# Kernel tuning notes

Measured on AMD Instinct MI355X. Metric: run time of the kernel, lower is better.

## Reference

```python
import jax, jax.numpy as jnp
import numpy as np

B, E, H, KVH, S = 1, 4096, 32, 8, 2048
HD = E // H            # per-head dim = 128
KVE = KVH * HD         # kv projection embed dim = 1024


def setup_inputs() -> dict:
    key = jax.random.key(0)
    ks = jax.random.split(key, 10)
    std = 0.02
    return {
        "input_embeds": jax.random.normal(ks[0], (B, E, 1, S), jnp.float32),
        "cos": jax.random.uniform(ks[1], (HD, S), jnp.float32, -1.0, 1.0),
        "sin": jax.random.uniform(ks[2], (HD, S), jnp.float32, -1.0, 1.0),
        "wq": jax.random.normal(ks[3], (E, E), jnp.float32) * std,
        "bq": jnp.zeros((E,), jnp.float32),
        "wk": jax.random.normal(ks[4], (KVE, E), jnp.float32) * std,
        "wv": jax.random.normal(ks[5], (KVE, E), jnp.float32) * std,
        "bv": jnp.zeros((KVE,), jnp.float32),
        "wo": jax.random.normal(ks[6], (E, E), jnp.float32) * std,
        "bo": jnp.zeros((E,), jnp.float32),
    }


def _proj(w, x, b=None):
    # 1x1 Conv2d == channelwise linear on (B, C, 1, S)
    y = jnp.einsum('oc,bcxs->boxs', w, x)
    if b is not None:
        y = y + b[None, :, None, None]
    return y


def _rope(x, cos, sin):
    # x: (B, h, HD, S); rotate-half along head_dim axis
    half = x.shape[2] // 2
    x1, x2 = x[:, :, :half], x[:, :, half:]
    rot = jnp.concatenate([-x2, x1], axis=2)
    return x * cos[None, None] + rot * sin[None, None]


def reference(input_embeds, cos, sin, wq, bq, wk, wv, bv, wo, bo):
    b, e, _, s = input_embeds.shape
    hd = e // H
    q = _proj(wq, input_embeds, bq)          # (B, E, 1, S)
    k = _proj(wk, input_embeds)              # (B, KVE, 1, S)  (no bias)
    v = _proj(wv, input_embeds, bv)          # (B, KVE, 1, S)

    qh = q.reshape(b, H, hd, s)
    kh = k.reshape(b, KVH, hd, s)
    qh = _rope(qh, cos, sin)
    kh = _rope(kh, cos, sin)

    # GQA tiling: channel-block repeat => query head h uses kv head (h % KVH)
    rep = H // KVH
    kfull = jnp.tile(kh, (1, rep, 1, 1))                       # (B, H, HD, S)
    vfull = jnp.tile(v.reshape(b, KVH, hd, s), (1, rep, 1, 1))  # (B, H, HD, S)

    scale = 1.0 / np.sqrt(hd).astype(np.float32)
    scores = jnp.einsum('bhcq,bhck->bhqk', qh, kfull) * scale  # (B, H, S, S)
    causal = jnp.tril(jnp.ones((s, s), bool))
    scores = jnp.where(causal[None, None], scores, jnp.finfo(scores.dtype).min)
    w = jax.nn.softmax(scores, axis=-1)
    attn = jnp.einsum('bhqk,bhck->bhcq', w, vfull).reshape(b, e, 1, s)
    return _proj(wo, attn, bo)
```

## Files before the change

### kernel.cpp

```cpp
#include <hip/hip_runtime.h>


typedef unsigned short u16;
typedef unsigned int u32;
typedef __attribute__((ext_vector_type(8))) short bf16x8;
typedef __attribute__((ext_vector_type(4))) float f32x4;

__device__ __forceinline__ u16 f2b(float f){
  union { float f; u32 u; } v; v.f = f;
  u32 r = (v.u + 0x7FFFu + ((v.u >> 16) & 1u)) >> 16;
  return (u16)r;
}
__device__ __forceinline__ float b2f(u16 b){
  union { u32 u; float f; } v; v.u = ((u32)b) << 16;
  return v.f;
}

__device__ __forceinline__ void gld16(const void* g, void* l){
  __builtin_amdgcn_global_load_lds((const __attribute__((address_space(1))) u32*)g,
                                   (__attribute__((address_space(3))) u32*)l, 16, 0, 0);
}

__global__ __launch_bounds__(256) void cvt_w(const float* __restrict__ src,
                                             u16* __restrict__ dst, int n4)
{
  int i = blockIdx.x * 256 + threadIdx.x;
  if (i < n4){
    float4 v = *(const float4*)&src[(size_t)i * 4];
    ushort4 o; o.x = f2b(v.x); o.y = f2b(v.y); o.z = f2b(v.z); o.w = f2b(v.w);
    *(ushort4*)&dst[(size_t)i * 4] = o;
  }
}

__global__ __launch_bounds__(256) void transpose_x(const float* __restrict__ X,
                                                   u16* __restrict__ XT)
{
  __shared__ float lds[64][65];
  const int c0 = blockIdx.x * 64, s0 = blockIdx.y * 64;
  const int tid = threadIdx.x;
  {
    const int sg = tid & 15, cl = tid >> 4;
#pragma unroll
    for (int p = 0; p < 4; ++p){
      int c = cl + p * 16;
      float4 v = *(const float4*)&X[(size_t)(c0 + c) * 2048 + s0 + sg * 4];
      lds[sg*4+0][c] = v.x; lds[sg*4+1][c] = v.y;
      lds[sg*4+2][c] = v.z; lds[sg*4+3][c] = v.w;
    }
  }
  __syncthreads();
  {
    const int cg = tid & 15, sl = tid >> 4;
#pragma unroll
    for (int p = 0; p < 4; ++p){
      int s = sl + p * 16;
      ushort4 o;
      o.x = f2b(lds[s][cg*4+0]); o.y = f2b(lds[s][cg*4+1]);
      o.z = f2b(lds[s][cg*4+2]); o.w = f2b(lds[s][cg*4+3]);
      *(ushort4*)&XT[(size_t)(s0 + s) * 4096 + c0 + cg * 4] = o;
    }
  }
}

template<int EPI, int ABF>
__global__ __launch_bounds__(256) void gemm2(
    const u16* __restrict__ W0, const u16* __restrict__ W1, const u16* __restrict__ W2,
    const float* __restrict__ F0, const float* __restrict__ F1, const float* __restrict__ F2,
    const u16* __restrict__ B,
    const float* __restrict__ bias0, const float* __restrict__ bias2,
    u16* __restrict__ QTo, u16* __restrict__ KTo, u16* __restrict__ Vno,
    float* __restrict__ OUT)
{
  const int K = 4096;
  const int m0 = blockIdx.y * 128, n0 = blockIdx.x * 128;

  const u16* A16; const float* Af; int mA;
  if (EPI == 0){
    if (m0 < 4096)      { A16 = W0; Af = F0; mA = m0; }
    else if (m0 < 5120) { A16 = W1; Af = F1; mA = m0 - 4096; }
    else                { A16 = W2; Af = F2; mA = m0 - 5120; }
  } else { A16 = W0; Af = F0; mA = m0; }

  __shared__ __align__(16) u16 As[128 * 32];
  __shared__ __align__(16) u16 Bs[128 * 32];

  const int tid = threadIdx.x, lane = tid & 63, w = tid >> 6;
  const int wm = w >> 1, wn = w & 1, quad = lane >> 4, l15 = lane & 15;

  f32x4 acc[4][4];
#pragma unroll
  for (int mt = 0; mt < 4; ++mt)
#pragma unroll
    for (int nt = 0; nt < 4; ++nt)
      acc[mt][nt] = f32x4{0.f, 0.f, 0.f, 0.f};

  const int r0 = tid >> 2, gs0 = tid & 3;
  const int g0 = gs0 ^ ((r0 >> 1) & 3);
  const int r1 = r0 + 64;

  u16* ldsA0 = As + (size_t)(w * 64) * 8;
  u16* ldsA1 = As + (size_t)(w * 64 + 256) * 8;
  u16* ldsB0 = Bs + (size_t)(w * 64) * 8;
  u16* ldsB1 = Bs + (size_t)(w * 64 + 256) * 8;

  const u16* bsrc0 = &B[(size_t)(n0 + r0) * 4096 + g0 * 8];
  const u16* bsrc1 = &B[(size_t)(n0 + r1) * 4096 + g0 * 8];
  const u16* asrc0 = ABF ? &A16[(size_t)(mA + r0) * 4096 + g0 * 8] : nullptr;
  const u16* asrc1 = ABF ? &A16[(size_t)(mA + r1) * 4096 + g0 * 8] : nullptr;
  const float* afs0 = ABF ? nullptr : &Af[(size_t)(mA + r0) * 4096 + g0 * 8];
  const float* afs1 = ABF ? nullptr : &Af[(size_t)(mA + r1) * 4096 + g0 * 8];

  int aoff[4], boff[4];
#pragma unroll
  for (int mt = 0; mt < 4; ++mt){
    int row = wm * 64 + mt * 16 + l15;
    aoff[mt] = row * 32 + (quad ^ ((row >> 1) & 3)) * 8;
  }
#pragma unroll
  for (int nt = 0; nt < 4; ++nt){
    int row = wn * 64 + nt * 16 + l15;
    boff[nt] = row * 32 + (quad ^ ((row >> 1) & 3)) * 8;
  }

  for (int kt = 0; kt < K / 32; ++kt){
    const int k0 = kt * 32;
    if (ABF){
      gld16(asrc0 + k0, ldsA0);
      gld16(asrc1 + k0, ldsA1);
    } else {
      float4 v0 = *(const float4*)&afs0[k0];
      float4 v1 = *(const float4*)&afs0[k0 + 4];
      float4 v2 = *(const float4*)&afs1[k0];
      float4 v3 = *(const float4*)&afs1[k0 + 4];
      union { u16 u[8]; uint4 q; } p0, p1;
      p0.u[0]=f2b(v0.x); p0.u[1]=f2b(v0.y); p0.u[2]=f2b(v0.z); p0.u[3]=f2b(v0.w);
      p0.u[4]=f2b(v1.x); p0.u[5]=f2b(v1.y); p0.u[6]=f2b(v1.z); p0.u[7]=f2b(v1.w);
      p1.u[0]=f2b(v2.x); p1.u[1]=f2b(v2.y); p1.u[2]=f2b(v2.z); p1.u[3]=f2b(v2.w);
      p1.u[4]=f2b(v3.x); p1.u[5]=f2b(v3.y); p1.u[6]=f2b(v3.z); p1.u[7]=f2b(v3.w);
      *(uint4*)&As[(size_t)tid * 8] = p0.q;
      *(uint4*)&As[(size_t)(tid + 256) * 8] = p1.q;
    }
    gld16(bsrc0 + k0, ldsB0);
    gld16(bsrc1 + k0, ldsB1);
    __syncthreads();

    bf16x8 af[4], bfr[4];
#pragma unroll
    for (int mt = 0; mt < 4; ++mt) af[mt]  = *(const bf16x8*)&As[aoff[mt]];
#pragma unroll
    for (int nt = 0; nt < 4; ++nt) bfr[nt] = *(const bf16x8*)&Bs[boff[nt]];
#pragma unroll
    for (int mt = 0; mt < 4; ++mt)
#pragma unroll
      for (int nt = 0; nt < 4; ++nt)
        acc[mt][nt] = __builtin_amdgcn_mfma_f32_16x16x32_bf16(af[mt], bfr[nt], acc[mt][nt], 0, 0, 0);
    __syncthreads();
  }

  if (EPI == 0){
    if (m0 < 4096){
#pragma unroll
      for (int mt = 0; mt < 4; ++mt){
        int mb = m0 + wm * 64 + mt * 16 + quad * 4;
        float b0 = bias0[mb], b1 = bias0[mb+1], b2 = bias0[mb+2], b3 = bias0[mb+3];
#pragma unroll
        for (int nt = 0; nt < 4; ++nt){
          int n = n0 + wn * 64 + nt * 16 + l15;
          ushort4 o;
          o.x = f2b(acc[mt][nt][0] + b0); o.y = f2b(acc[mt][nt][1] + b1);
          o.z = f2b(acc[mt][nt][2] + b2); o.w = f2b(acc[mt][nt][3] + b3);
          *(ushort4*)&QTo[(size_t)n * 4096 + mb] = o;
        }
      }
    } else if (m0 < 5120){
#pragma unroll
      for (int mt = 0; mt < 4; ++mt){
        int mb = m0 - 4096 + wm * 64 + mt * 16 + quad * 4;
#pragma unroll
        for (int nt = 0; nt < 4; ++nt){
          int n = n0 + wn * 64 + nt * 16 + l15;
          ushort4 o;
          o.x = f2b(acc[mt][nt][0]); o.y = f2b(acc[mt][nt][1]);
          o.z = f2b(acc[mt][nt][2]); o.w = f2b(acc[mt][nt][3]);
          *(ushort4*)&KTo[(size_t)n * 1024 + mb] = o;
        }
      }
    } else {
#pragma unroll
      for (int mt = 0; mt < 4; ++mt)
#pragma unroll
        for (int r = 0; r < 4; ++r){
          int mv = m0 - 5120 + wm * 64 + mt * 16 + quad * 4 + r;
          float bb = bias2[mv];
#pragma unroll
          for (int nt = 0; nt < 4; ++nt){
            int n = n0 + wn * 64 + nt * 16 + l15;
            Vno[(size_t)mv * 2048 + n] = f2b(acc[mt][nt][r] + bb);
          }
        }
    }
  } else {
#pragma unroll
    for (int mt = 0; mt < 4; ++mt)
#pragma unroll
      for (int r = 0; r < 4; ++r){
        int m = m0 + wm * 64 + mt * 16 + quad * 4 + r;
        float bb = bias0[m];
#pragma unroll
        for (int nt = 0; nt < 4; ++nt){
          int n = n0 + wn * 64 + nt * 16 + l15;
          OUT[(size_t)m * 2048 + n] = acc[mt][nt][r] + bb;
        }
      }
  }
}

__global__ __launch_bounds__(256) void rope_kernel(u16* __restrict__ QT,
                                                   u16* __restrict__ KT,
                                                   const float* __restrict__ cosp,
                                                   const float* __restrict__ sinp)
{
  const float qscale = 0.08838834764831845f * 1.4426950408889634f;
  int gid = blockIdx.x * 256 + threadIdx.x;
  const int NQ = 2048 * 32 * 64;
  if (gid < NQ){
    int c = gid & 63, hh = (gid >> 6) & 31, s = gid >> 11;
    size_t base = (size_t)s * 4096 + hh * 128 + c;
    float x1 = b2f(QT[base]), x2 = b2f(QT[base + 64]);
    float c1 = cosp[c * 2048 + s],        s1 = sinp[c * 2048 + s];
    float c2 = cosp[(c + 64) * 2048 + s], s2 = sinp[(c + 64) * 2048 + s];
    QT[base]      = f2b((x1 * c1 - x2 * s1) * qscale);
    QT[base + 64] = f2b((x2 * c2 + x1 * s2) * qscale);
  } else {
    int g = gid - NQ;
    int c = g & 63, hh = (g >> 6) & 7, s = g >> 9;
    size_t base = (size_t)s * 1024 + hh * 128 + c;
    float x1 = b2f(KT[base]), x2 = b2f(KT[base + 64]);
    float c1 = cosp[c * 2048 + s],        s1 = sinp[c * 2048 + s];
    float c2 = cosp[(c + 64) * 2048 + s], s2 = sinp[(c + 64) * 2048 + s];
    KT[base]      = f2b(x1 * c1 - x2 * s1);
    KT[base + 64] = f2b(x2 * c2 + x1 * s2);
  }
}

__global__ __launch_bounds__(256, 1) void attn3(const u16* __restrict__ QT,
                                                const u16* __restrict__ KT,
                                                const u16* __restrict__ Vn,
                                                u16* __restrict__ AT)
{
  const int h = blockIdx.x;
  const int p = blockIdx.y;
  const int kvh = h & 7;
  const int tid = threadIdx.x;
  const int w = tid >> 6, lane = tid & 63;
  const int quad = lane >> 4, l15 = lane & 15;

  const int k  = 4 * p + w;
  const int t1 = k, t2 = 63 - k;
  const int e1 = t1 >> 1, e2 = t2 >> 1;
  const int i01 = t1 * 32, i02 = t2 * 32;
  const int U = 32 - 2 * p;

  __shared__ __align__(16) u16 Ks[2][64 * 128];
  __shared__ __align__(16) u16 Vs[128 * 64];
  __shared__ __align__(16) u16 Ps[4][16][64];

  bf16x8 qa1[2][4], qa2[2][4];
#pragma unroll
  for (int mt = 0; mt < 2; ++mt)
#pragma unroll
    for (int kc = 0; kc < 4; ++kc){
      qa1[mt][kc] = *(const bf16x8*)&QT[(size_t)(i01 + mt * 16 + l15) * 4096
                                        + h * 128 + kc * 32 + quad * 8];
      qa2[mt][kc] = *(const bf16x8*)&QT[(size_t)(i02 + mt * 16 + l15) * 4096
                                        + h * 128 + kc * 32 + quad * 8];
    }

  f32x4 o1[2][9], o2[2][9];
#pragma unroll
  for (int mt = 0; mt < 2; ++mt)
#pragma unroll
    for (int ct = 0; ct < 9; ++ct){
      o1[mt][ct] = f32x4{0.f, 0.f, 0.f, 0.f};
      o2[mt][ct] = f32x4{0.f, 0.f, 0.f, 0.f};
    }

  bf16x8 ones;
#pragma unroll
  for (int z = 0; z < 8; ++z) ones[z] = (short)0x3F80;

  const int krl = lane >> 4, kgl = lane & 15;
  const int vrl = lane >> 3, vgl = lane & 7;

  auto stageK = [&](int buf, int j0){
#pragma unroll
    for (int q = 0; q < 4; ++q){
      int r = w * 16 + q * 4 + krl;
      gld16(&KT[(size_t)(j0 + r) * 1024 + kvh * 128 + ((kgl ^ (r & 7)) * 8)],
            &Ks[buf][(size_t)(w * 16 + q * 4) * 128]);
    }
  };
  auto stageV = [&](int j0){
#pragma unroll
    for (int q = 0; q < 4; ++q){
      int r = w * 32 + q * 8 + vrl;
      gld16(&Vn[(size_t)(kvh * 128 + r) * 2048 + j0 + ((vgl ^ (r & 7)) * 8)],
            &Vs[(size_t)(w * 32 + q * 8) * 64]);
    }
  };

  auto soft = [&](f32x4 (&s)[2][4], bf16x8 (&pa)[2][2], f32x4 (&o)[2][9],
                  int i0, int j0, bool maskit){
#pragma unroll
    for (int mt = 0; mt < 2; ++mt){
#pragma unroll
      for (int nt = 0; nt < 4; ++nt)
#pragma unroll
        for (int r = 0; r < 4; ++r){
          float pv = exp2f(fminf(s[mt][nt][r], 60.0f));
          if (maskit && (j0 + nt * 16 + l15 > i0 + mt * 16 + quad * 4 + r)) pv = 0.0f;
          int col = nt * 16 + l15, rowp = quad * 4 + r;
          Ps[w][rowp][((col >> 3) ^ (rowp & 7)) * 8 + (col & 7)] = f2b(pv);
        }
#pragma unroll
      for (int kc = 0; kc < 2; ++kc){
        pa[mt][kc] = *(const bf16x8*)&Ps[w][l15][((kc * 4 + quad) ^ (l15 & 7)) * 8];
        o[mt][8] = __builtin_amdgcn_mfma_f32_16x16x32_bf16(pa[mt][kc], ones, o[mt][8], 0, 0, 0);
      }
    }
  };

  auto epilogue = [&](f32x4 (&o)[2][9], int i0){
#pragma unroll
    for (int mt = 0; mt < 2; ++mt){
      float rinv[4];
#pragma unroll
      for (int r = 0; r < 4; ++r) rinv[r] = 1.0f / o[mt][8][r];
#pragma unroll
      for (int ct = 0; ct < 8; ++ct)
#pragma unroll
        for (int r = 0; r < 4; ++r){
          int i = i0 + mt * 16 + quad * 4 + r;
          AT[(size_t)i * 4096 + h * 128 + ct * 16 + l15] = f2b(o[mt][ct][r] * rinv[r]);
        }
    }
  };

  stageK(0, 0);
  for (int u = 0; u < U; ++u){
    __syncthreads();
    if (u + 1 < U) stageK((u + 1) & 1, (u + 1) * 64);
    stageV(u * 64);

    const int j0 = u * 64;
    const bool act1 = (u <= e1), act2 = (u <= e2);
    const u16* Kb = &Ks[u & 1][0];

    f32x4 s1[2][4], s2[2][4];
    bf16x8 pa1[2][2], pa2[2][2];
    if (act2 || act1){
#pragma unroll
      for (int mt = 0; mt < 2; ++mt)
#pragma unroll
        for (int nt = 0; nt < 4; ++nt){
          s1[mt][nt] = f32x4{0.f, 0.f, 0.f, 0.f};
          s2[mt][nt] = f32x4{0.f, 0.f, 0.f, 0.f};
        }
#pragma unroll
      for (int nt = 0; nt < 4; ++nt){
        bf16x8 kb[4];
#pragma unroll
        for (int kc = 0; kc < 4; ++kc){
          int row = nt * 16 + l15;
          kb[kc] = *(const bf16x8*)&Kb[row * 128 + (((kc * 4 + quad) ^ (row & 7)) * 8)];
        }
#pragma unroll
        for (int kc = 0; kc < 4; ++kc){
          s2[0][nt] = __builtin_amdgcn_mfma_f32_16x16x32_bf16(qa2[0][kc], kb[kc], s2[0][nt], 0, 0, 0);
          s2[1][nt] = __builtin_amdgcn_mfma_f32_16x16x32_bf16(qa2[1][kc], kb[kc], s2[1][nt], 0, 0, 0);
        }
        if (act1)
#pragma unroll
          for (int kc = 0; kc < 4; ++kc){
            s1[0][nt] = __builtin_amdgcn_mfma_f32_16x16x32_bf16(qa1[0][kc], kb[kc], s1[0][nt], 0, 0, 0);
            s1[1][nt] = __builtin_amdgcn_mfma_f32_16x16x32_bf16(qa1[1][kc], kb[kc], s1[1][nt], 0, 0, 0);
          }
      }
      if (act2) soft(s2, pa2, o2, i02, j0, u == e2);
      if (act1) soft(s1, pa1, o1, i01, j0, u == e1);
    }
    __syncthreads();

    if (act2 || act1){
#pragma unroll
      for (int ct = 0; ct < 8; ++ct)
#pragma unroll
        for (int kc = 0; kc < 2; ++kc){
          int row = ct * 16 + l15;
          bf16x8 vb = *(const bf16x8*)&Vs[row * 64 + (((kc * 4 + quad) ^ (row & 7)) * 8)];
          if (act2){
            o2[0][ct] = __builtin_amdgcn_mfma_f32_16x16x32_bf16(pa2[0][kc], vb, o2[0][ct], 0, 0, 0);
            o2[1][ct] = __builtin_amdgcn_mfma_f32_16x16x32_bf16(pa2[1][kc], vb, o2[1][ct], 0, 0, 0);
          }
          if (act1){
            o1[0][ct] = __builtin_amdgcn_mfma_f32_16x16x32_bf16(pa1[0][kc], vb, o1[0][ct], 0, 0, 0);
            o1[1][ct] = __builtin_amdgcn_mfma_f32_16x16x32_bf16(pa1[1][kc], vb, o1[1][ct], 0, 0, 0);
          }
        }
      if (u == e2) epilogue(o2, i02);
      if (u == e1) epilogue(o1, i01);
    }
  }
}

extern "C" void kernel_launch(void* const* d_in, const int* in_sizes, int n_in,
                              void* d_out, int out_size, void* d_ws, size_t ws_size,
                              hipStream_t stream)
{
  const float* X    = (const float*)d_in[0];
  const float* cosp = (const float*)d_in[1];
  const float* sinp = (const float*)d_in[2];
  const float* wq   = (const float*)d_in[3];
  const float* bq   = (const float*)d_in[4];
  const float* wk   = (const float*)d_in[5];
  const float* wv   = (const float*)d_in[6];
  const float* bv   = (const float*)d_in[7];
  const float* wo   = (const float*)d_in[8];
  const float* bo   = (const float*)d_in[9];
  float* out = (float*)d_out;

  char* ws = (char*)d_ws;
  const size_t MB = 1u << 20;

  if (ws_size >= 88 * MB){
    u16* W16Q = (u16*)(ws);
    u16* W16K = (u16*)(ws + 32 * MB);
    u16* W16V = (u16*)(ws + 40 * MB);
    u16* XT   = (u16*)(ws + 48 * MB);
    u16* QT   = (u16*)(ws + 64 * MB);
    u16* KT   = (u16*)(ws + 80 * MB);
    u16* Vn   = (u16*)(ws + 84 * MB);
    u16* AT   = (u16*)(ws + 48 * MB);
    u16* WO16 = (u16*)(ws);

    cvt_w<<<16384, 256, 0, stream>>>(wq, W16Q, 4194304);
    cvt_w<<< 4096, 256, 0, stream>>>(wk, W16K, 1048576);
    cvt_w<<< 4096, 256, 0, stream>>>(wv, W16V, 1048576);
    transpose_x<<<dim3(64, 32), 256, 0, stream>>>(X, XT);
    gemm2<0,1><<<dim3(16, 48), 256, 0, stream>>>(W16Q, W16K, W16V, wq, wk, wv,
                                                 XT, bq, bv, QT, KT, Vn, nullptr);
    cvt_w<<<16384, 256, 0, stream>>>(wo, WO16, 4194304);
    rope_kernel<<<20480, 256, 0, stream>>>(QT, KT, cosp, sinp);
    attn3<<<dim3(32, 8), 256, 0, stream>>>(QT, KT, Vn, AT);
    gemm2<1,1><<<dim3(16, 32), 256, 0, stream>>>(WO16, nullptr, nullptr, wo, nullptr, nullptr,
                                                 AT, bo, nullptr, nullptr, nullptr, nullptr, out);
  } else {
    u16* XT = (u16*)(ws);
    u16* QT = (u16*)(ws + 16 * MB);
    u16* KT = (u16*)(ws + 32 * MB);
    u16* Vn = (u16*)(ws + 36 * MB);
    u16* AT = (u16*)(ws + 40 * MB);

    transpose_x<<<dim3(64, 32), 256, 0, stream>>>(X, XT);
    gemm2<0,0><<<dim3(16, 48), 256, 0, stream>>>(nullptr, nullptr, nullptr, wq, wk, wv,
                                                 XT, bq, bv, QT, KT, Vn, nullptr);
    rope_kernel<<<20480, 256, 0, stream>>>(QT, KT, cosp, sinp);
    attn3<<<dim3(32, 8), 256, 0, stream>>>(QT, KT, Vn, AT);
    gemm2<1,0><<<dim3(16, 32), 256, 0, stream>>>(nullptr, nullptr, nullptr, wo, nullptr, nullptr,
                                                 AT, bo, nullptr, nullptr, nullptr, nullptr, out);
  }
}
```

Baseline: 662.8 us.

## Add 256x256-tile 512-thread bf16 GEMM with double-buffered LDS for projections

Adds a new GEMM kernel with 256x256 output tiles, 8 waves, and a 64-wide K step split into two 32-wide halves. Global-to-LDS loads are double-buffered and overlapped with MFMA through explicit vmcnt waits and barriers, with wave priority raised around the MFMA blocks. The QKV and output projections on the large-workspace path use this kernel in place of the 128-tile gemm2. Each tile reuses more data from memory, but the kernel needs much more LDS and many accumulator registers. Only 192 and 128 blocks are launched, which may underfill the GPU.

Result: no change. 673.1 us (+1.6%).

```diff
diff --git a/kernel.cpp b/kernel.cpp
--- a/kernel.cpp
+++ b/kernel.cpp
@@ -205,6 +205,172 @@
 #pragma unroll
       for (int r = 0; r < 4; ++r){
         int m = m0 + wm * 64 + mt * 16 + quad * 4 + r;
+        float bb = bias0[m];
+#pragma unroll
+        for (int nt = 0; nt < 4; ++nt){
+          int n = n0 + wn * 64 + nt * 16 + l15;
+          OUT[(size_t)m * 2048 + n] = acc[mt][nt][r] + bb;
+        }
+      }
+  }
+}
+
+template<int EPI>
+__global__ __launch_bounds__(512, 2) void gemm256(
+    const u16* __restrict__ W0, const u16* __restrict__ W1, const u16* __restrict__ W2,
+    const u16* __restrict__ Bmat,
+    const float* __restrict__ bias0, const float* __restrict__ bias2,
+    u16* __restrict__ QTo, u16* __restrict__ KTo, u16* __restrict__ Vno,
+    float* __restrict__ OUT)
+{
+  const int NT = 64;
+  const int m0 = blockIdx.y * 256, n0 = blockIdx.x * 256;
+
+  const u16* A16; int mA;
+  if (EPI == 0){
+    if (m0 < 4096)      { A16 = W0; mA = m0; }
+    else if (m0 < 5120) { A16 = W1; mA = m0 - 4096; }
+    else                { A16 = W2; mA = m0 - 5120; }
+  } else { A16 = W0; mA = m0; }
+
+  __shared__ __align__(16) u16 As[2 * 2 * 8192];
+  __shared__ __align__(16) u16 Bs[2 * 2 * 8192];
+
+  const int tid = threadIdx.x, lane = tid & 63, w = tid >> 6;
+  const int wm = w >> 2, wn = w & 3, quad = lane >> 4, l15 = lane & 15;
+
+  f32x4 acc[8][4];
+#pragma unroll
+  for (int mt = 0; mt < 8; ++mt)
+#pragma unroll
+    for (int nt = 0; nt < 4; ++nt)
+      acc[mt][nt] = f32x4{0.f, 0.f, 0.f, 0.f};
+
+  const int rowq = tid >> 2;
+  const int kg   = (tid & 3) * 8;
+  const u16* aG = &A16[(size_t)(mA + rowq) * 4096 + kg];
+  const u16* bG = &Bmat[(size_t)(n0 + rowq) * 4096 + kg];
+  u16* AsW = As + w * 512;
+  u16* BsW = Bs + w * 512;
+
+  int aoff[8], boff[4];
+#pragma unroll
+  for (int mt = 0; mt < 8; ++mt) aoff[mt] = (wm * 128 + mt * 16 + l15) * 32 + quad * 8;
+#pragma unroll
+  for (int nt = 0; nt < 4; ++nt) boff[nt] = (wn * 64 + nt * 16 + l15) * 32 + quad * 8;
+
+  auto stage8 = [&](int b, int k0){
+    u16* Ad = AsW + b * 16384;
+    u16* Bd = BsW + b * 16384;
+    const u16* as_ = aG + k0;
+    const u16* bs_ = bG + k0;
+    gld16(as_,                   Ad);
+    gld16(as_ + 128 * 4096,      Ad + 4096);
+    gld16(bs_,                   Bd);
+    gld16(bs_ + 128 * 4096,      Bd + 4096);
+    gld16(as_ + 32,              Ad + 8192);
+    gld16(as_ + 32 + 128 * 4096, Ad + 8192 + 4096);
+    gld16(bs_ + 32,              Bd + 8192);
+    gld16(bs_ + 32 + 128 * 4096, Bd + 8192 + 4096);
+  };
+
+  stage8(0, 0);
+  asm volatile("s_waitcnt vmcnt(4)" ::: "memory");
+  __builtin_amdgcn_s_barrier();
+  __builtin_amdgcn_sched_barrier(0);
+
+#pragma unroll 1
+  for (int t = 0; t < NT; ++t){
+    const int buf = t & 1;
+    const u16* Asl = As + buf * 16384;
+    const u16* Bsl = Bs + buf * 16384;
+
+    {
+      bf16x8 af[8], bf[4];
+#pragma unroll
+      for (int mt = 0; mt < 8; ++mt) af[mt] = *(const bf16x8*)&Asl[aoff[mt]];
+#pragma unroll
+      for (int nt = 0; nt < 4; ++nt) bf[nt] = *(const bf16x8*)&Bsl[boff[nt]];
+      if (t + 1 < NT) stage8((t + 1) & 1, (t + 1) * 64);
+      __builtin_amdgcn_s_setprio(1);
+#pragma unroll
+      for (int mt = 0; mt < 8; ++mt)
+#pragma unroll
+        for (int nt = 0; nt < 4; ++nt)
+          acc[mt][nt] = __builtin_amdgcn_mfma_f32_16x16x32_bf16(af[mt], bf[nt], acc[mt][nt], 0, 0, 0);
+      __builtin_amdgcn_s_setprio(0);
+      if (t + 1 < NT) { asm volatile("s_waitcnt vmcnt(8)" ::: "memory"); }
+      else            { asm volatile("s_waitcnt vmcnt(0)" ::: "memory"); }
+      __builtin_amdgcn_s_barrier();
+      __builtin_amdgcn_sched_barrier(0);
+    }
+    {
+      bf16x8 af[8], bf[4];
+#pragma unroll
+      for (int mt = 0; mt < 8; ++mt) af[mt] = *(const bf16x8*)&Asl[8192 + aoff[mt]];
+#pragma unroll
+      for (int nt = 0; nt < 4; ++nt) bf[nt] = *(const bf16x8*)&Bsl[8192 + boff[nt]];
+      __builtin_amdgcn_s_setprio(1);
+#pragma unroll
+      for (int mt = 0; mt < 8; ++mt)
+#pragma unroll
+        for (int nt = 0; nt < 4; ++nt)
+          acc[mt][nt] = __builtin_amdgcn_mfma_f32_16x16x32_bf16(af[mt], bf[nt], acc[mt][nt], 0, 0, 0);
+      __builtin_amdgcn_s_setprio(0);
+      if (t + 1 < NT) { asm volatile("s_waitcnt vmcnt(4)" ::: "memory"); }
+      __builtin_amdgcn_s_barrier();
+      __builtin_amdgcn_sched_barrier(0);
+    }
+  }
+
+  if (EPI == 0){
+    if (m0 < 4096){
+#pragma unroll
+      for (int mt = 0; mt < 8; ++mt){
+        int mb = m0 + wm * 128 + mt * 16 + quad * 4;
+        float b0 = bias0[mb], b1 = bias0[mb+1], b2 = bias0[mb+2], b3 = bias0[mb+3];
+#pragma unroll
+        for (int nt = 0; nt < 4; ++nt){
+          int n = n0 + wn * 64 + nt * 16 + l15;
+          ushort4 o;
+          o.x = f2b(acc[mt][nt][0] + b0); o.y = f2b(acc[mt][nt][1] + b1);
+          o.z = f2b(acc[mt][nt][2] + b2); o.w = f2b(acc[mt][nt][3] + b3);
+          *(ushort4*)&QTo[(size_t)n * 4096 + mb] = o;
+        }
+      }
+    } else if (m0 < 5120){
+#pragma unroll
+      for (int mt = 0; mt < 8; ++mt){
+        int mb = m0 - 4096 + wm * 128 + mt * 16 + quad * 4;
+#pragma unroll
+        for (int nt = 0; nt < 4; ++nt){
+          int n = n0 + wn * 64 + nt * 16 + l15;
+          ushort4 o;
+          o.x = f2b(acc[mt][nt][0]); o.y = f2b(acc[mt][nt][1]);
+          o.z = f2b(acc[mt][nt][2]); o.w = f2b(acc[mt][nt][3]);
+          *(ushort4*)&KTo[(size_t)n * 1024 + mb] = o;
+        }
+      }
+    } else {
+#pragma unroll
+      for (int mt = 0; mt < 8; ++mt)
+#pragma unroll
+        for (int r = 0; r < 4; ++r){
+          int mv = m0 - 5120 + wm * 128 + mt * 16 + quad * 4 + r;
+          float bb = bias2[mv];
+#pragma unroll
+          for (int nt = 0; nt < 4; ++nt){
+            int n = n0 + wn * 64 + nt * 16 + l15;
+            Vno[(size_t)mv * 2048 + n] = f2b(acc[mt][nt][r] + bb);
+          }
+        }
+    }
+  } else {
+#pragma unroll
+    for (int mt = 0; mt < 8; ++mt)
+#pragma unroll
+      for (int r = 0; r < 4; ++r){
+        int m = m0 + wm * 128 + mt * 16 + quad * 4 + r;
         float bb = bias0[m];
 #pragma unroll
         for (int nt = 0; nt < 4; ++nt){
@@ -447,13 +613,13 @@
     cvt_w<<< 4096, 256, 0, stream>>>(wk, W16K, 1048576);
     cvt_w<<< 4096, 256, 0, stream>>>(wv, W16V, 1048576);
     transpose_x<<<dim3(64, 32), 256, 0, stream>>>(X, XT);
-    gemm2<0,1><<<dim3(16, 48), 256, 0, stream>>>(W16Q, W16K, W16V, wq, wk, wv,
-                                                 XT, bq, bv, QT, KT, Vn, nullptr);
+    gemm256<0><<<dim3(8, 24), 512, 0, stream>>>(W16Q, W16K, W16V, XT,
+                                                bq, bv, QT, KT, Vn, nullptr);
     cvt_w<<<16384, 256, 0, stream>>>(wo, WO16, 4194304);
     rope_kernel<<<20480, 256, 0, stream>>>(QT, KT, cosp, sinp);
     attn3<<<dim3(32, 8), 256, 0, stream>>>(QT, KT, Vn, AT);
-    gemm2<1,1><<<dim3(16, 32), 256, 0, stream>>>(WO16, nullptr, nullptr, wo, nullptr, nullptr,
-                                                 AT, bo, nullptr, nullptr, nullptr, nullptr, out);
+    gemm256<1><<<dim3(8, 16), 512, 0, stream>>>(WO16, nullptr, nullptr, AT,
+                                                bo, nullptr, nullptr, nullptr, nullptr, out);
   } else {
     u16* XT = (u16*)(ws);
     u16* QT = (u16*)(ws + 16 * MB);
```
